# Optimization experiments

Measured on AMD Instinct MI355X. Metric: run time of the kernel, lower is better.

The kernel has to match this reference:

```python
import jax, jax.numpy as jnp
import numpy as np

REG_MAX = 16
NC = 80
TOPK = 10
ALPHA = 1.0
BETA = 6.0
BOX_W, CLS_W, DFL_W = 7.5, 0.5, 1.5
IMG = 1280.0


def _ciou(b1, b2, eps=1e-7):
    # b1, b2: [..., 4] xyxy, broadcastable
    b1x1, b1y1, b1x2, b1y2 = b1[..., 0], b1[..., 1], b1[..., 2], b1[..., 3]
    b2x1, b2y1, b2x2, b2y2 = b2[..., 0], b2[..., 1], b2[..., 2], b2[..., 3]
    w1, h1 = b1x2 - b1x1, b1y2 - b1y1
    w2, h2 = b2x2 - b2x1, b2y2 - b2y1
    inter = (jnp.maximum(jnp.minimum(b1x2, b2x2) - jnp.maximum(b1x1, b2x1), 0.0) *
             jnp.maximum(jnp.minimum(b1y2, b2y2) - jnp.maximum(b1y1, b2y1), 0.0))
    union = w1 * h1 + w2 * h2 - inter + eps
    iou = inter / union
    cw = jnp.maximum(b1x2, b2x2) - jnp.minimum(b1x1, b2x1)
    ch = jnp.maximum(b1y2, b2y2) - jnp.minimum(b1y1, b2y1)
    c2 = cw * cw + ch * ch + eps
    rho2 = ((b2x1 + b2x2 - b1x1 - b1x2) ** 2 + (b2y1 + b2y2 - b1y1 - b1y2) ** 2) / 4.0
    v = (4.0 / np.pi ** 2) * (jnp.arctan(w2 / (h2 + eps)) - jnp.arctan(w1 / (h1 + eps))) ** 2
    alpha = jax.lax.stop_gradient(v / (v - iou + (1.0 + eps)))
    return iou - (rho2 / c2 + v * alpha)


def _loss(p0, p1, p2, gt_boxes, gt_labels, strides):
    preds = [p0, p1, p2]
    B = p0.shape[0]
    aps, sts, pds, pcs = [], [], [], []
    for i, p in enumerate(preds):
        H, W = p.shape[2], p.shape[3]
        gy, gx = jnp.meshgrid(jnp.arange(H, dtype=p.dtype) + 0.5,
                              jnp.arange(W, dtype=p.dtype) + 0.5, indexing='ij')
        aps.append(jnp.stack([gx.ravel(), gy.ravel()], -1))          # [HW,2] feat units
        sts.append(jnp.ones((H * W, 1), p.dtype) * strides[i])       # [HW,1]
        pds.append(p[:, :4 * REG_MAX].reshape(B, 4, REG_MAX, H * W).transpose(0, 3, 1, 2))
        pcs.append(p[:, 4 * REG_MAX:].transpose(0, 2, 3, 1).reshape(B, H * W, NC))
    ap = jnp.concatenate(aps)                 # [N,2]
    st = jnp.concatenate(sts)                 # [N,1]
    pred_dist = jnp.concatenate(pds, axis=1)  # [B,N,4,R]
    pred_cls = jnp.concatenate(pcs, axis=1)   # [B,N,NC]
    proj = jnp.arange(REG_MAX, dtype=p0.dtype)
    M = gt_boxes.shape[1]
    N = ap.shape[0]

    def one_image(pd, pc, gb, gl):
        # decode boxes (image units)
        dist = jnp.einsum('nkr,r->nk', jax.nn.softmax(pd, -1), proj)        # [N,4]
        pred_boxes = jnp.concatenate([(ap - dist[:, :2]) * st,
                                      (ap + dist[:, 2:]) * st], -1)          # [N,4]
        # ---- TaskAlignedAssigner (no grad) ----
        sg = jax.lax.stop_gradient
        pb, ps, gbs = sg(pred_boxes), sg(jax.nn.sigmoid(pc)), sg(gb)
        ap_img = ap * st                                                     # [N,2]
        in_gt = ((ap_img[:, None, 0] >= gbs[None, :, 0]) & (ap_img[:, None, 0] <= gbs[None, :, 2]) &
                 (ap_img[:, None, 1] >= gbs[None, :, 1]) & (ap_img[:, None, 1] <= gbs[None, :, 3]))
        ious = jnp.maximum(_ciou(pb[:, None, :], gbs[None, :, :]), 0.0)      # [N,M]
        align = (ps[:, gl] ** ALPHA) * (ious ** BETA) * in_gt
        align = align / (align.max(0, keepdims=True) + 1e-9)
        align = align * (ious > 0.1)
        # topk anchors per GT; anchor takes the GT with max masked score
        #  sequential loop with strict '>' updates)
        vals, idx = jax.lax.top_k(align.T, TOPK)                             # [M,TOPK]
        masked = jnp.zeros((M, N), align.dtype).at[
            jnp.arange(M)[:, None], idx].set(jnp.where(vals > 0, vals, 0.0))
        col = masked.T                                                       # [N,M]
        best_gt = jnp.argmax(col, 1)
        best_score = col.max(1)
        fg = (best_score > 0).astype(pd.dtype)                               # [N]
        num_fg = jnp.maximum(fg.sum(), 1.0)
        labels = gl[best_gt]
        boxes = gbs[best_gt]
        # ---- box (CIoU) loss over fg ----
        box_loss = ((1.0 - _ciou(pred_boxes, boxes)) * fg).sum() / num_fg
        # ---- DFL loss over fg ----
        t = jnp.concatenate([ap - boxes[:, :2] / st, boxes[:, 2:] / st - ap], -1)
        t = jnp.clip(t, 0.0, REG_MAX - 1 - 0.01)   # box2dist clamp
        t = jnp.clip(t, 0.0, REG_MAX - 1e-4)       # DFLLoss clamp
        left = jnp.floor(t).astype(jnp.int32)
        right = jnp.minimum(left + 1, REG_MAX - 1)
        wl = right.astype(t.dtype) - t
        wr = t - left.astype(t.dtype)
        logp = jax.nn.log_softmax(pd, -1)                                    # [N,4,R]
        ce_l = -jnp.take_along_axis(logp, left[..., None], -1)[..., 0]
        ce_r = -jnp.take_along_axis(logp, right[..., None], -1)[..., 0]
        dfl_loss = ((ce_l * wl + ce_r * wr) * fg[:, None]).sum() / (num_fg * 4.0)
        # ---- cls BCE-with-logits over all anchors ----
        cls_t = jax.nn.one_hot(labels, NC, dtype=pc.dtype) * (best_score * fg)[:, None]
        cls_loss = (jnp.logaddexp(0.0, pc) - pc * cls_t).sum(1).mean()
        has_fg = (fg.sum() > 0).astype(pd.dtype)
        return box_loss * has_fg, cls_loss * has_fg, dfl_loss * has_fg

    bl, cl, dl = jax.vmap(one_image)(pred_dist, pred_cls, gt_boxes, gt_labels)
    return BOX_W * bl.sum() + CLS_W * cl.sum() + DFL_W * dl.sum()


def setup_inputs() -> dict:
    key = jax.random.key(0)
    ks = jax.random.split(key, 6)
    p0 = jax.random.normal(ks[0], (8, 144, 160, 160), jnp.float32)
    p1 = jax.random.normal(ks[1], (8, 144, 80, 80), jnp.float32)
    p2 = jax.random.normal(ks[2], (8, 144, 40, 40), jnp.float32)
    cxcy = jax.random.uniform(ks[3], (8, 32, 2), minval=64.0, maxval=IMG - 64.0)
    wh = jax.random.uniform(ks[4], (8, 32, 2), minval=16.0, maxval=256.0)
    gt_boxes = jnp.clip(jnp.concatenate([cxcy - wh / 2, cxcy + wh / 2], -1), 0.0, IMG)
    gt_labels = jax.random.randint(ks[5], (8, 32), 0, NC)
    strides = jnp.array([8.0, 16.0, 32.0], jnp.float32)
    return {"p0": p0, "p1": p1, "p2": p2, "gt_boxes": gt_boxes,
            "gt_labels": gt_labels, "strides": strides}


def reference(p0, p1, p2, gt_boxes, gt_labels, strides):
    return _loss(p0, p1, p2, gt_boxes, gt_labels, strides)
```

## Files before the change

### kernel.cpp

```cpp
#include <hip/hip_runtime.h>
#include <cstdint>

#define NANCHOR 33600
#define BATCH   8
#define MGT     32
#define NCLS    80
#define MAXFG   (BATCH * MGT * 10)

struct AInfo {
    const float* ch0;
    int   hw;
    float apx, apy, st;
};

__device__ __forceinline__ AInfo anchor_info(const float* p0, const float* p1,
                                             const float* p2, int b, int n) {
    AInfo r;
    if (n < 25600) {
        int nn = n;
        r.ch0 = p0 + (size_t)b * (144 * 25600) + nn;
        r.hw = 25600; r.st = 8.f;
        r.apx = (float)(nn % 160) + 0.5f;
        r.apy = (float)(nn / 160) + 0.5f;
    } else if (n < 32000) {
        int nn = n - 25600;
        r.ch0 = p1 + (size_t)b * (144 * 6400) + nn;
        r.hw = 6400; r.st = 16.f;
        r.apx = (float)(nn % 80) + 0.5f;
        r.apy = (float)(nn / 80) + 0.5f;
    } else {
        int nn = n - 32000;
        r.ch0 = p2 + (size_t)b * (144 * 1600) + nn;
        r.hw = 1600; r.st = 32.f;
        r.apx = (float)(nn % 40) + 0.5f;
        r.apy = (float)(nn / 40) + 0.5f;
    }
    return r;
}

__device__ __forceinline__ float ciou_f(float b1x1, float b1y1, float b1x2, float b1y2,
                                        float g1x, float g1y, float g2x, float g2y) {
    const float eps = 1e-7f;
    float w1 = b1x2 - b1x1, h1 = b1y2 - b1y1;
    float w2 = g2x - g1x,   h2 = g2y - g1y;
    float iw = fminf(b1x2, g2x) - fmaxf(b1x1, g1x);
    float ih = fminf(b1y2, g2y) - fmaxf(b1y1, g1y);
    float inter = fmaxf(iw, 0.f) * fmaxf(ih, 0.f);
    float uni = w1 * h1 + w2 * h2 - inter + eps;
    float iou = inter / uni;
    float cw = fmaxf(b1x2, g2x) - fminf(b1x1, g1x);
    float ch = fmaxf(b1y2, g2y) - fminf(b1y1, g1y);
    float c2 = cw * cw + ch * ch + eps;
    float dx = g1x + g2x - b1x1 - b1x2;
    float dy = g1y + g2y - b1y1 - b1y2;
    float rho2 = (dx * dx + dy * dy) * 0.25f;
    float t = atanf(w2 / (h2 + eps)) - atanf(w1 / (h1 + eps));
    float v = 0.40528473456935108577f * t * t;
    float alpha = v / (v - iou + (1.f + eps));
    return iou - (rho2 / c2 + v * alpha);
}

__device__ __forceinline__ float4 max4(float4 a, float4 b) {
    return make_float4(fmaxf(a.x, b.x), fmaxf(a.y, b.y), fmaxf(a.z, b.z), fmaxf(a.w, b.w));
}
__device__ __forceinline__ float fast_splus(float x) {
    return fmaxf(x, 0.f) + __logf(1.f + __expf(-fabsf(x)));
}


__global__ void k_init(float* acc) {
    acc[threadIdx.x] = 0.f;
}

__global__ __launch_bounds__(128) void k_decode(const float* __restrict__ p0,
                                                const float* __restrict__ p1,
                                                const float* __restrict__ p2,
                                                float2* __restrict__ pb2,
                                                unsigned long long* __restrict__ best,
                                                float* __restrict__ acc) {
    int b = blockIdx.y;
    int role = blockIdx.z;
    int t = blockIdx.x * 128 + threadIdx.x;

    if (role >= 2) {
        float sp = 0.f;
        if (t < NANCHOR / 4) {
            int n = t * 4;
            const float* ch0; int hw;
            if (n < 25600)      { ch0 = p0 + (size_t)b * (144 * 25600) + n;          hw = 25600; }
            else if (n < 32000) { ch0 = p1 + (size_t)b * (144 * 6400) + (n - 25600); hw = 6400; }
            else                { ch0 = p2 + (size_t)b * (144 * 1600) + (n - 32000); hw = 1600; }
            int c0 = 64 + (role - 2) * 40;
#pragma unroll 8
            for (int c = 0; c < 40; c++) {
                float4 x = *(const float4*)(ch0 + (size_t)(c0 + c) * hw);
                sp += fast_splus(x.x) + fast_splus(x.y) + fast_splus(x.z) + fast_splus(x.w);
            }
        }
#pragma unroll
        for (int o = 32; o > 0; o >>= 1) sp += __shfl_down(sp, o, 64);
        if ((threadIdx.x & 63) == 0) atomicAdd(&acc[b * 8 + 0], sp);
        return;
    }

    if (t >= NANCHOR / 4) return;
    int n = t * 4;
    const float* ch0; int hw; float st, apx, apy;
    if (n < 25600) {
        ch0 = p0 + (size_t)b * (144 * 25600) + n;
        hw = 25600; st = 8.f;
        apx = (float)(n % 160) + 0.5f; apy = (float)(n / 160) + 0.5f;
    } else if (n < 32000) {
        int nn = n - 25600;
        ch0 = p1 + (size_t)b * (144 * 6400) + nn;
        hw = 6400; st = 16.f;
        apx = (float)(nn % 80) + 0.5f; apy = (float)(nn / 80) + 0.5f;
    } else {
        int nn = n - 32000;
        ch0 = p2 + (size_t)b * (144 * 1600) + nn;
        hw = 1600; st = 32.f;
        apx = (float)(nn % 40) + 0.5f; apy = (float)(nn / 40) + 0.5f;
    }

    int k0 = role * 2;
    float d[2][4];
#pragma unroll
    for (int kk = 0; kk < 2; kk++) {
        float4 v[16];
#pragma unroll
        for (int r = 0; r < 16; r++)
            v[r] = *(const float4*)(ch0 + (size_t)((k0 + kk) * 16 + r) * hw);
        float4 mx = v[0];
#pragma unroll
        for (int r = 1; r < 16; r++) mx = max4(mx, v[r]);
        float4 s  = make_float4(0.f, 0.f, 0.f, 0.f);
        float4 sw = make_float4(0.f, 0.f, 0.f, 0.f);
#pragma unroll
        for (int r = 0; r < 16; r++) {
            float fr = (float)r;
            float ex = __expf(v[r].x - mx.x);
            float ey = __expf(v[r].y - mx.y);
            float ez = __expf(v[r].z - mx.z);
            float ew = __expf(v[r].w - mx.w);
            s.x += ex; s.y += ey; s.z += ez; s.w += ew;
            sw.x += ex * fr; sw.y += ey * fr; sw.z += ez * fr; sw.w += ew * fr;
        }
        d[kk][0] = sw.x / s.x; d[kk][1] = sw.y / s.y;
        d[kk][2] = sw.z / s.z; d[kk][3] = sw.w / s.w;
    }

    size_t base = (size_t)b * NANCHOR + n;
    if (role == 0) {
#pragma unroll
        for (int i = 0; i < 4; i++) {
            float ax = apx + (float)i;
            pb2[(base + i) * 2 + 0] = make_float2((ax - d[0][i]) * st, (apy - d[1][i]) * st);
        }
#pragma unroll
        for (int i = 0; i < 4; i++) best[base + i] = 0ull;
    } else {
#pragma unroll
        for (int i = 0; i < 4; i++) {
            float ax = apx + (float)i;
            pb2[(base + i) * 2 + 1] = make_float2((ax + d[0][i]) * st, (apy + d[1][i]) * st);
        }
    }
}

__global__ __launch_bounds__(256) void k_assign(const float* __restrict__ p0,
                                                const float* __restrict__ p1,
                                                const float* __restrict__ p2,
                                                const float4* __restrict__ pb,
                                                const float* __restrict__ gtb,
                                                const int* __restrict__ gtl,
                                                unsigned long long* __restrict__ best,
                                                float* __restrict__ acc,
                                                uint2* __restrict__ fglist) {
    int bm = blockIdx.x;
    int b = bm >> 5, m = bm & 31;
    const float* g = gtb + (size_t)(b * MGT + m) * 4;
    float g0 = g[0], g1 = g[1], g2 = g[2], g3 = g[3];
    int label = gtl[b * MGT + m];
    int tid = threadIdx.x;

    float tv[10];
    int   ti[10];
#pragma unroll
    for (int j = 0; j < 10; j++) { tv[j] = -1.f; ti[j] = 0x7fffffff; }
    float maxu = 0.f;

    const int   LW[3]   = {160, 80, 40};
    const int   LOFF[3] = {0, 25600, 32000};
    const float LST[3]  = {8.f, 16.f, 32.f};

    for (int l = 0; l < 3; l++) {
        float st = LST[l];
        int W = LW[l];
        float inv_st = 1.f / st;
        int ix0 = max(0,     (int)floorf(g0 * inv_st - 0.5f) - 1);
        int ix1 = min(W - 1, (int)ceilf (g2 * inv_st - 0.5f) + 1);
        int iy0 = max(0,     (int)floorf(g1 * inv_st - 0.5f) - 1);
        int iy1 = min(W - 1, (int)ceilf (g3 * inv_st - 0.5f) + 1);
        int nx = ix1 - ix0 + 1, ny = iy1 - iy0 + 1;
        if (nx <= 0 || ny <= 0) continue;
        int cnt = nx * ny;
        const float* lp = (l == 0) ? p0 : (l == 1) ? p1 : p2;
        int hw = W * W;
        const float* ch0 = lp + (size_t)b * 144 * hw;
        const float* pcls = ch0 + (size_t)(64 + label) * hw;

        for (int idx = tid; idx < cnt; idx += 256) {
            int iy = iy0 + idx / nx;
            int ix = ix0 + idx % nx;
            float ax = ((float)ix + 0.5f) * st;
            float ay = ((float)iy + 0.5f) * st;
            if (ax < g0 || ax > g2 || ay < g1 || ay > g3) continue;
            int nn = iy * W + ix;
            int n = LOFF[l] + nn;
            float4 box = pb[(size_t)b * NANCHOR + n];
            float c = ciou_f(box.x, box.y, box.z, box.w, g0, g1, g2, g3);
            float iou = fmaxf(c, 0.f);
            if (iou <= 0.f) continue;
            float pcv = pcls[nn];
            float ps = 1.f / (1.f + __expf(-pcv));
            float i2 = iou * iou;
            float a = ps * i2 * i2 * i2;
            maxu = fmaxf(maxu, a);
            if (iou > 0.1f && a > tv[9]) {
                tv[9] = a; ti[9] = n;
#pragma unroll
                for (int j = 9; j > 0; --j) {
                    if (tv[j] > tv[j - 1]) {
                        float tf = tv[j]; tv[j] = tv[j - 1]; tv[j - 1] = tf;
                        int   tt = ti[j]; ti[j] = ti[j - 1]; ti[j - 1] = tt;
                    }
                }
            }
        }
    }

    __shared__ float sval[2560];
    __shared__ int   sidx[2560];
    __shared__ float rv[256];
    __shared__ int   ra[256];
    __shared__ int   rs[256];
    __shared__ float smax[256];
    __shared__ int   winners[10];
    __shared__ int   nwin;

#pragma unroll
    for (int j = 0; j < 10; j++) {
        sval[tid * 10 + j] = tv[j];
        sidx[tid * 10 + j] = ti[j];
    }
    smax[tid] = maxu;
    if (tid == 0) nwin = 0;
    __syncthreads();
    for (int s = 128; s > 0; s >>= 1) {
        if (tid < s) smax[tid] = fmaxf(smax[tid], smax[tid + s]);
        __syncthreads();
    }
    float denom = smax[0] + 1e-9f;

    for (int r = 0; r < 10; r++) {
        float bv = -1.f; int ba = 0x7fffffff; int bs = -1;
#pragma unroll
        for (int j = 0; j < 10; j++) {
            int s0 = tid * 10 + j;
            float v = sval[s0]; int a0 = sidx[s0];
            if (v > bv || (v == bv && a0 < ba)) { bv = v; ba = a0; bs = s0; }
        }
        rv[tid] = bv; ra[tid] = ba; rs[tid] = bs;
        __syncthreads();
        for (int s = 128; s > 0; s >>= 1) {
            if (tid < s) {
                if (rv[tid + s] > rv[tid] ||
                    (rv[tid + s] == rv[tid] && ra[tid + s] < ra[tid])) {
                    rv[tid] = rv[tid + s]; ra[tid] = ra[tid + s]; rs[tid] = rs[tid + s];
                }
            }
            __syncthreads();
        }
        if (tid == 0 && rv[0] > 0.f) {
            float nv = rv[0] / denom;
            unsigned long long pk =
                ((unsigned long long)__float_as_uint(nv) << 32) |
                (unsigned long long)(31 - m);
            atomicMax(&best[(size_t)b * NANCHOR + ra[0]], pk);
            winners[nwin++] = ra[0];
            sval[rs[0]] = -1.f;
        }
        __syncthreads();
    }

    if (tid == 0 && nwin > 0) {
        unsigned int* list_cnt = (unsigned int*)(acc + 120);
        unsigned int base = atomicAdd(list_cnt, (unsigned int)nwin);
        for (int j = 0; j < nwin; j++)
            fglist[base + j] = make_uint2((unsigned int)(b * NANCHOR + winners[j]),
                                          (unsigned int)m);
    }
}

__global__ __launch_bounds__(256) void k_final(const float* __restrict__ p0,
                                               const float* __restrict__ p1,
                                               const float* __restrict__ p2,
                                               const float4* __restrict__ pb,
                                               const float* __restrict__ gtb,
                                               const int* __restrict__ gtl,
                                               const unsigned long long* __restrict__ best,
                                               const uint2* __restrict__ fglist,
                                               float* __restrict__ acc) {
    __shared__ float sacc[BATCH][4];
    int tid = threadIdx.x;
    if (tid < BATCH * 4) sacc[tid >> 2][tid & 3] = 0.f;
    __syncthreads();

    unsigned int cnt = *(const unsigned int*)(acc + 120);
    unsigned int i = blockIdx.x * 256 + tid;
    if (i < cnt) {
        uint2 e = fglist[i];
        int bn = (int)e.x, m = (int)e.y;
        unsigned long long pk = best[bn];
        if ((unsigned int)(pk & 0xffffffffull) == (unsigned int)(31 - m)) {
            int b = bn / NANCHOR, n = bn % NANCHOR;
            float score = __uint_as_float((unsigned int)(pk >> 32));
            const float* g = gtb + (size_t)(b * MGT + m) * 4;
            float g0 = g[0], g1 = g[1], g2 = g[2], g3 = g[3];
            int label = gtl[b * MGT + m];
            float4 box = pb[bn];
            float c = ciou_f(box.x, box.y, box.z, box.w, g0, g1, g2, g3);

            AInfo ai = anchor_info(p0, p1, p2, b, n);
            float inv_st = 1.f / ai.st;
            float t4[4] = { ai.apx - g0 * inv_st, ai.apy - g1 * inv_st,
                            g2 * inv_st - ai.apx, g3 * inv_st - ai.apy };
            float dfl = 0.f;
#pragma unroll
            for (int k = 0; k < 4; k++) {
                float t = fminf(fmaxf(t4[k], 0.f), 14.99f);
                int left = (int)floorf(t);
                int right = (left + 1 < 15) ? left + 1 : 15;
                float wl = (float)right - t;
                float wr = t - (float)left;
                float v[16];
                float mx = -1e30f;
#pragma unroll
                for (int r = 0; r < 16; r++) {
                    v[r] = ai.ch0[(size_t)(k * 16 + r) * ai.hw];
                    mx = fmaxf(mx, v[r]);
                }
                float s = 0.f;
#pragma unroll
                for (int r = 0; r < 16; r++) s += __expf(v[r] - mx);
                float lse = mx + __logf(s);
                dfl += (lse - v[left]) * wl + (lse - v[right]) * wr;
            }
            float pcv = ai.ch0[(size_t)(64 + label) * ai.hw];

            atomicAdd(&sacc[b][0], 1.f - c);
            atomicAdd(&sacc[b][1], dfl);
            atomicAdd(&sacc[b][2], pcv * score);
            atomicAdd(&sacc[b][3], 1.f);
        }
    }
    __syncthreads();
    if (tid < BATCH * 4) {
        float v = sacc[tid >> 2][tid & 3];
        if (v != 0.f) atomicAdd(&acc[(tid >> 2) * 8 + 1 + (tid & 3)], v);
    }
}

__global__ void k_combine(const float* __restrict__ acc, float* __restrict__ out) {
    if (blockIdx.x == 0 && threadIdx.x == 0) {
        float total = 0.f;
        for (int b = 0; b < BATCH; b++) {
            float nfr = acc[b * 8 + 4];
            float has = nfr > 0.f ? 1.f : 0.f;
            float nf = fmaxf(nfr, 1.f);
            float box_l = acc[b * 8 + 1] / nf;
            float cls_l = (acc[b * 8 + 0] - acc[b * 8 + 3]) / (float)NANCHOR;
            float dfl_l = acc[b * 8 + 2] / (nf * 4.f);
            total += has * (7.5f * box_l + 0.5f * cls_l + 1.5f * dfl_l);
        }
        out[0] = total;
    }
}

extern "C" void kernel_launch(void* const* d_in, const int* in_sizes, int n_in,
                              void* d_out, int out_size, void* d_ws, size_t ws_size,
                              hipStream_t stream) {
    (void)in_sizes; (void)n_in; (void)out_size; (void)ws_size;
    const float* p0  = (const float*)d_in[0];
    const float* p1  = (const float*)d_in[1];
    const float* p2  = (const float*)d_in[2];
    const float* gtb = (const float*)d_in[3];
    const int*   gtl = (const int*)d_in[4];

    char* ws = (char*)d_ws;
    unsigned long long* best = (unsigned long long*)ws;
    float4* pb = (float4*)(ws + (size_t)BATCH * NANCHOR * 8);
    float*  acc = (float*)(ws + (size_t)BATCH * NANCHOR * 8
                              + (size_t)BATCH * NANCHOR * 16);
    uint2* fglist = (uint2*)((char*)acc + 512);

    k_init   <<<1, 128, 0, stream>>>(acc);
    k_decode <<<dim3(66, BATCH, 4), 128, 0, stream>>>(p0, p1, p2, (float2*)pb, best, acc);
    k_assign <<<BATCH * MGT, 256, 0, stream>>>(p0, p1, p2, pb, gtb, gtl, best, acc, fglist);
    k_final  <<<(MAXFG + 255) / 256, 256, 0, stream>>>(p0, p1, p2, pb, gtb, gtl, best,
                                                       fglist, acc);
    k_combine<<<1, 64, 0, stream>>>(acc, (float*)d_out);
}
```

Before: 266.2 us.

## Split softplus over more blocks, drop softmax max pass, parallelize DFL per side

The class softplus reduction is spread over four z-roles of 20 channels each, using four independent accumulators. The distribution decode fuses both sides into one loop and drops the max-subtraction pass from the softmax. The final loss kernel assigns four threads per foreground entry, one per box side, so each DFL side is computed in parallel. Skipping the max subtraction removes a pass and lowers register pressure, but it risks exp overflow for large logits.

Measured after the change: 254.3 us. -4.5%, faster.

```diff
diff --git a/kernel.cpp b/kernel.cpp
--- a/kernel.cpp
+++ b/kernel.cpp
@@ -60,11 +60,11 @@
     return iou - (rho2 / c2 + v * alpha);
 }
 
-__device__ __forceinline__ float4 max4(float4 a, float4 b) {
-    return make_float4(fmaxf(a.x, b.x), fmaxf(a.y, b.y), fmaxf(a.z, b.z), fmaxf(a.w, b.w));
-}
 __device__ __forceinline__ float fast_splus(float x) {
     return fmaxf(x, 0.f) + __logf(1.f + __expf(-fabsf(x)));
+}
+__device__ __forceinline__ float sp4(float4 x) {
+    return fast_splus(x.x) + fast_splus(x.y) + fast_splus(x.z) + fast_splus(x.w);
 }
 
 
@@ -83,20 +83,24 @@
     int t = blockIdx.x * 128 + threadIdx.x;
 
     if (role >= 2) {
-        float sp = 0.f;
+        float s0 = 0.f, s1 = 0.f, s2 = 0.f, s3 = 0.f;
         if (t < NANCHOR / 4) {
             int n = t * 4;
             const float* ch0; int hw;
             if (n < 25600)      { ch0 = p0 + (size_t)b * (144 * 25600) + n;          hw = 25600; }
             else if (n < 32000) { ch0 = p1 + (size_t)b * (144 * 6400) + (n - 25600); hw = 6400; }
             else                { ch0 = p2 + (size_t)b * (144 * 1600) + (n - 32000); hw = 1600; }
-            int c0 = 64 + (role - 2) * 40;
-#pragma unroll 8
-            for (int c = 0; c < 40; c++) {
-                float4 x = *(const float4*)(ch0 + (size_t)(c0 + c) * hw);
-                sp += fast_splus(x.x) + fast_splus(x.y) + fast_splus(x.z) + fast_splus(x.w);
+            const float* cp = ch0 + (size_t)(64 + (role - 2) * 20) * hw;
+#pragma unroll
+            for (int c = 0; c < 20; c += 4) {
+                float4 x0 = *(const float4*)(cp + (size_t)(c + 0) * hw);
+                float4 x1 = *(const float4*)(cp + (size_t)(c + 1) * hw);
+                float4 x2 = *(const float4*)(cp + (size_t)(c + 2) * hw);
+                float4 x3 = *(const float4*)(cp + (size_t)(c + 3) * hw);
+                s0 += sp4(x0); s1 += sp4(x1); s2 += sp4(x2); s3 += sp4(x3);
             }
         }
+        float sp = (s0 + s1) + (s2 + s3);
 #pragma unroll
         for (int o = 32; o > 0; o >>= 1) sp += __shfl_down(sp, o, 64);
         if ((threadIdx.x & 63) == 0) atomicAdd(&acc[b * 8 + 0], sp);
@@ -123,38 +127,32 @@
     }
 
     int k0 = role * 2;
-    float d[2][4];
-#pragma unroll
-    for (int kk = 0; kk < 2; kk++) {
-        float4 v[16];
-#pragma unroll
-        for (int r = 0; r < 16; r++)
-            v[r] = *(const float4*)(ch0 + (size_t)((k0 + kk) * 16 + r) * hw);
-        float4 mx = v[0];
-#pragma unroll
-        for (int r = 1; r < 16; r++) mx = max4(mx, v[r]);
-        float4 s  = make_float4(0.f, 0.f, 0.f, 0.f);
-        float4 sw = make_float4(0.f, 0.f, 0.f, 0.f);
-#pragma unroll
-        for (int r = 0; r < 16; r++) {
-            float fr = (float)r;
-            float ex = __expf(v[r].x - mx.x);
-            float ey = __expf(v[r].y - mx.y);
-            float ez = __expf(v[r].z - mx.z);
-            float ew = __expf(v[r].w - mx.w);
-            s.x += ex; s.y += ey; s.z += ez; s.w += ew;
-            sw.x += ex * fr; sw.y += ey * fr; sw.z += ez * fr; sw.w += ew * fr;
-        }
-        d[kk][0] = sw.x / s.x; d[kk][1] = sw.y / s.y;
-        d[kk][2] = sw.z / s.z; d[kk][3] = sw.w / s.w;
-    }
+    const float* cA = ch0 + (size_t)(k0 * 16) * hw;
+    const float* cB = cA + (size_t)16 * hw;
+    float4 sA = make_float4(0.f, 0.f, 0.f, 0.f), wA = sA, sB = sA, wB = sA;
+#pragma unroll
+    for (int r = 0; r < 16; r++) {
+        float4 a = *(const float4*)(cA + (size_t)r * hw);
+        float4 c = *(const float4*)(cB + (size_t)r * hw);
+        float fr = (float)r;
+        float eax = __expf(a.x), eay = __expf(a.y), eaz = __expf(a.z), eaw = __expf(a.w);
+        float ecx = __expf(c.x), ecy = __expf(c.y), ecz = __expf(c.z), ecw = __expf(c.w);
+        sA.x += eax; sA.y += eay; sA.z += eaz; sA.w += eaw;
+        sB.x += ecx; sB.y += ecy; sB.z += ecz; sB.w += ecw;
+        wA.x = fmaf(eax, fr, wA.x); wA.y = fmaf(eay, fr, wA.y);
+        wA.z = fmaf(eaz, fr, wA.z); wA.w = fmaf(eaw, fr, wA.w);
+        wB.x = fmaf(ecx, fr, wB.x); wB.y = fmaf(ecy, fr, wB.y);
+        wB.z = fmaf(ecz, fr, wB.z); wB.w = fmaf(ecw, fr, wB.w);
+    }
+    float dA[4] = { wA.x / sA.x, wA.y / sA.y, wA.z / sA.z, wA.w / sA.w };
+    float dB[4] = { wB.x / sB.x, wB.y / sB.y, wB.z / sB.z, wB.w / sB.w };
 
     size_t base = (size_t)b * NANCHOR + n;
     if (role == 0) {
 #pragma unroll
         for (int i = 0; i < 4; i++) {
             float ax = apx + (float)i;
-            pb2[(base + i) * 2 + 0] = make_float2((ax - d[0][i]) * st, (apy - d[1][i]) * st);
+            pb2[(base + i) * 2 + 0] = make_float2((ax - dA[i]) * st, (apy - dB[i]) * st);
         }
 #pragma unroll
         for (int i = 0; i < 4; i++) best[base + i] = 0ull;
@@ -162,7 +160,7 @@
 #pragma unroll
         for (int i = 0; i < 4; i++) {
             float ax = apx + (float)i;
-            pb2[(base + i) * 2 + 1] = make_float2((ax + d[0][i]) * st, (apy + d[1][i]) * st);
+            pb2[(base + i) * 2 + 1] = make_float2((ax + dA[i]) * st, (apy + dB[i]) * st);
         }
     }
 }
@@ -317,51 +315,52 @@
     __syncthreads();
 
     unsigned int cnt = *(const unsigned int*)(acc + 120);
-    unsigned int i = blockIdx.x * 256 + tid;
+    unsigned int j = blockIdx.x * 256 + tid;
+    unsigned int i = j >> 2;
+    int k = (int)(j & 3);
     if (i < cnt) {
         uint2 e = fglist[i];
         int bn = (int)e.x, m = (int)e.y;
         unsigned long long pk = best[bn];
         if ((unsigned int)(pk & 0xffffffffull) == (unsigned int)(31 - m)) {
             int b = bn / NANCHOR, n = bn % NANCHOR;
-            float score = __uint_as_float((unsigned int)(pk >> 32));
             const float* g = gtb + (size_t)(b * MGT + m) * 4;
             float g0 = g[0], g1 = g[1], g2 = g[2], g3 = g[3];
-            int label = gtl[b * MGT + m];
-            float4 box = pb[bn];
-            float c = ciou_f(box.x, box.y, box.z, box.w, g0, g1, g2, g3);
-
             AInfo ai = anchor_info(p0, p1, p2, b, n);
             float inv_st = 1.f / ai.st;
-            float t4[4] = { ai.apx - g0 * inv_st, ai.apy - g1 * inv_st,
-                            g2 * inv_st - ai.apx, g3 * inv_st - ai.apy };
-            float dfl = 0.f;
-#pragma unroll
-            for (int k = 0; k < 4; k++) {
-                float t = fminf(fmaxf(t4[k], 0.f), 14.99f);
-                int left = (int)floorf(t);
-                int right = (left + 1 < 15) ? left + 1 : 15;
-                float wl = (float)right - t;
-                float wr = t - (float)left;
-                float v[16];
-                float mx = -1e30f;
-#pragma unroll
-                for (int r = 0; r < 16; r++) {
-                    v[r] = ai.ch0[(size_t)(k * 16 + r) * ai.hw];
-                    mx = fmaxf(mx, v[r]);
-                }
-                float s = 0.f;
-#pragma unroll
-                for (int r = 0; r < 16; r++) s += __expf(v[r] - mx);
-                float lse = mx + __logf(s);
-                dfl += (lse - v[left]) * wl + (lse - v[right]) * wr;
+            float tk = (k == 0) ? ai.apx - g0 * inv_st
+                     : (k == 1) ? ai.apy - g1 * inv_st
+                     : (k == 2) ? g2 * inv_st - ai.apx
+                     :            g3 * inv_st - ai.apy;
+            float t = fminf(fmaxf(tk, 0.f), 14.99f);
+            int left = (int)floorf(t);
+            int right = (left + 1 < 15) ? left + 1 : 15;
+            float wl = (float)right - t;
+            float wr = t - (float)left;
+            float v[16];
+            float mx = -1e30f;
+#pragma unroll
+            for (int r = 0; r < 16; r++) {
+                v[r] = ai.ch0[(size_t)(k * 16 + r) * ai.hw];
+                mx = fmaxf(mx, v[r]);
             }
-            float pcv = ai.ch0[(size_t)(64 + label) * ai.hw];
-
-            atomicAdd(&sacc[b][0], 1.f - c);
+            float s = 0.f;
+#pragma unroll
+            for (int r = 0; r < 16; r++) s += __expf(v[r] - mx);
+            float lse = mx + __logf(s);
+            float dfl = (lse - v[left]) * wl + (lse - v[right]) * wr;
             atomicAdd(&sacc[b][1], dfl);
-            atomicAdd(&sacc[b][2], pcv * score);
-            atomicAdd(&sacc[b][3], 1.f);
+
+            if (k == 0) {
+                float score = __uint_as_float((unsigned int)(pk >> 32));
+                int label = gtl[b * MGT + m];
+                float4 box = pb[bn];
+                float c = ciou_f(box.x, box.y, box.z, box.w, g0, g1, g2, g3);
+                float pcv = ai.ch0[(size_t)(64 + label) * ai.hw];
+                atomicAdd(&sacc[b][0], 1.f - c);
+                atomicAdd(&sacc[b][2], pcv * score);
+                atomicAdd(&sacc[b][3], 1.f);
+            }
         }
     }
     __syncthreads();
@@ -405,9 +404,9 @@
     uint2* fglist = (uint2*)((char*)acc + 512);
 
     k_init   <<<1, 128, 0, stream>>>(acc);
-    k_decode <<<dim3(66, BATCH, 4), 128, 0, stream>>>(p0, p1, p2, (float2*)pb, best, acc);
+    k_decode <<<dim3(66, BATCH, 6), 128, 0, stream>>>(p0, p1, p2, (float2*)pb, best, acc);
     k_assign <<<BATCH * MGT, 256, 0, stream>>>(p0, p1, p2, pb, gtb, gtl, best, acc, fglist);
-    k_final  <<<(MAXFG + 255) / 256, 256, 0, stream>>>(p0, p1, p2, pb, gtb, gtl, best,
-                                                       fglist, acc);
+    k_final  <<<(MAXFG * 4 + 255) / 256, 256, 0, stream>>>(p0, p1, p2, pb, gtb, gtl, best,
+                                                           fglist, acc);
     k_combine<<<1, 64, 0, stream>>>(acc, (float*)d_out);
 }
```
